# Kernel tuning notes

Hardware: AMD Instinct MI355X
Metric: run time of the kernel (lower is better)

The kernel has to match this reference:

```python
import jax, jax.numpy as jnp
import numpy as np
from jax import lax

B, T, N, E, H = 8, 12, 716, 10, 64
DIN = 1 + H  # GCN input dim = x(1) concat state(H)
CS = 1       # conv_steps (predict_time)


def setup_inputs() -> dict:
    key = jax.random.key(0)
    ks = jax.random.split(key, 26)
    def rn(i, shape, s=0.1):
        return jax.random.normal(ks[i], shape, jnp.float32) * s
    data = jax.random.normal(ks[0], (B, T, N, 1), jnp.float32)
    tid = jax.random.uniform(ks[1], (B, T, N, 1), jnp.float32)          # time-of-day in [0,1)
    diw = jax.random.randint(ks[2], (B, T, N, 1), 0, 7).astype(jnp.float32)  # day-of-week
    source = jnp.concatenate([data, tid, diw], axis=-1)
    return dict(
        source=source,
        node_embeddings=rn(3, (N, E), 1.0),
        tid_emb=rn(4, (288, E), 1.0),
        diw_emb=rn(5, (7, E), 1.0),
        wp_g=rn(6, (2, E, 2, DIN, 2 * H)),
        bp_g=rn(7, (2, E, 2 * H)),
        fc1W_g=rn(8, (2, 16, DIN)), fc1b_g=rn(9, (2, 16)),
        fc2W_g=rn(10, (2, 2, 16)), fc2b_g=rn(11, (2, 2)),
        fc3W_g=rn(12, (2, E, 2)), fc3b_g=rn(13, (2, E)),
        wp_u=rn(14, (2, E, 2, DIN, H)),
        bp_u=rn(15, (2, E, H)),
        fc1W_u=rn(16, (2, 16, DIN)), fc1b_u=rn(17, (2, 16)),
        fc2W_u=rn(18, (2, 2, 16)), fc2b_u=rn(19, (2, 2)),
        fc3W_u=rn(20, (2, E, 2)), fc3b_u=rn(21, (2, E)),
        predW=rn(22, (2, T, CS, H)),
        predB=rn(23, (2, T)),
        skipW=rn(24, (T, CS, H)),
        skipB=rn(25, (T,)),
    )


def _gcn(x, emb_t, static, wp, bp, fc):
    # x: [B,N,DIN], emb_t: [B,N,E], static: [N,E]
    fc1W, fc1b, fc2W, fc2b, fc3W, fc3b = fc
    h = jax.nn.sigmoid(x @ fc1W.T + fc1b)
    h = jax.nn.sigmoid(h @ fc2W.T + fc2b)
    x_ = h @ fc3W.T + fc3b                            # [B,N,E]
    nodevec = jnp.tanh(emb_t * x_)                    # [B,N,E]
    graph = jax.nn.relu(jnp.einsum('bne,bme->bnm', nodevec, nodevec))
    d = jnp.sum(graph, axis=-1) ** -0.5               # [B,N]
    L = d[:, :, None] * graph * d[:, None, :]         # D^-1/2 A D^-1/2 support
    xg2 = jnp.einsum('bnm,bmc->bnc', L, x)
    w = jnp.einsum('ne,ekio->nkio', static, wp)       # [N,2,DIN,out]
    b = static @ bp                                   # [N,out]
    # support1 is identity -> x_g1 == x
    return (jnp.einsum('bni,nio->bno', x, w[:, 0])
            + jnp.einsum('bni,nio->bno', xg2, w[:, 1]) + b)


def _gru_layer(x_seq, emb_seq, static, gate_p, upd_p):
    # x_seq: [T,B,N,1], emb_seq: [T,B,N,E]
    wp_g, bp_g, fc_g = gate_p
    wp_u, bp_u, fc_u = upd_p
    Hd = wp_u.shape[-1]
    def step(state, inp):
        x, emb = inp
        xs = jnp.concatenate([x, state], axis=-1)
        zr = jax.nn.sigmoid(_gcn(xs, emb, static, wp_g, bp_g, fc_g))
        z, r = jnp.split(zr, 2, axis=-1)
        cand = jnp.concatenate([x, z * state], axis=-1)
        hc = jnp.tanh(_gcn(cand, emb, static, wp_u, bp_u, fc_u))
        h = r * state + (1 - r) * hc
        return h, h
    h0 = jnp.zeros(x_seq.shape[1:3] + (Hd,), x_seq.dtype)
    _, hs = lax.scan(step, h0, (x_seq, emb_seq))
    return hs  # [T,B,N,H]


def reference(source, node_embeddings, tid_emb, diw_emb,
              wp_g, bp_g, fc1W_g, fc1b_g, fc2W_g, fc2b_g, fc3W_g, fc3b_g,
              wp_u, bp_u, fc1W_u, fc1b_u, fc2W_u, fc2b_u, fc3W_u, fc3b_u,
              predW, predB, skipW, skipB):
    x = source[..., :1]                                   # [B,T,N,1]
    tid_idx = (source[..., 1] * 288).astype(jnp.int32)
    diw_idx = source[..., 2].astype(jnp.int32)
    emb = node_embeddings * tid_emb[tid_idx] * diw_emb[diw_idx]  # [B,T,N,E]
    x_t = jnp.moveaxis(x, 1, 0)                           # [T,B,N,1]
    emb_t = jnp.moveaxis(emb, 1, 0)                       # [T,B,N,E]
    cur = x_t
    predict = jnp.zeros((x.shape[0], T, x.shape[2], 1), x.dtype)
    for c in range(2):  # two structurally distinct GRU layers
        gate_p = (wp_g[c], bp_g[c], (fc1W_g[c], fc1b_g[c], fc2W_g[c], fc2b_g[c], fc3W_g[c], fc3b_g[c]))
        upd_p = (wp_u[c], bp_u[c], (fc1W_u[c], fc1b_u[c], fc2W_u[c], fc2b_u[c], fc3W_u[c], fc3b_u[c]))
        hs = _gru_layer(cur, emb_t, node_embeddings, gate_p, upd_p)
        ci = jnp.moveaxis(hs[-CS:], 0, 1)                 # [B,CS,N,H] (dropout is identity in eval)
        out = jnp.einsum('bcnh,och->bon', ci, predW[c]) + predB[c][None, :, None]
        predict = predict + out[..., None]                # [B,T,N,1]
        if c == 0:
            sk = jnp.einsum('bcnh,och->bon', ci, skipW) + skipB[None, :, None]
            cur = x_t - jnp.moveaxis(sk[..., None], 1, 0)
    return predict
```

## Files before the change

### kernel.cpp

```cpp
#include <hip/hip_runtime.h>
#include <math.h>

#define BB 8
#define TT 12
#define NN 716
#define EE 10
#define HH 64
#define DIN 65
#define OG 128
#define OU 64
#define XSP 68
#define JS 12
#define JRX 60
#define NTN 128
#define NP 768
#define NI4 17

__device__ __forceinline__ float sigmf(float x){ return 1.0f/(1.0f+__expf(-x)); }

__global__ void k_emb(const float* __restrict__ src, const float* __restrict__ ne,
                      const float* __restrict__ te, const float* __restrict__ de,
                      float* __restrict__ emb, float* __restrict__ cur){
  int idx = blockIdx.x*256 + threadIdx.x;
  if (idx >= BB*TT*NN) return;
  int n = idx % NN; int t = (idx/NN) % TT; int b = idx/(NN*TT);
  const float* s = src + (size_t)idx*3;
  float x = s[0];
  int ti = (int)(s[1]*288.0f);
  int di = (int)(s[2]);
  size_t eo = ((size_t)b*TT + t)*NN*EE + (size_t)n*EE;
  #pragma unroll
  for (int e=0;e<EE;e++)
    emb[eo+e] = ne[n*EE+e]*te[ti*EE+e]*de[di*EE+e];
  cur[((size_t)t*BB + b)*NN + n] = x;
}

__global__ __launch_bounds__(256) void k_prep_w4m(
    const float* __restrict__ ne, const float* __restrict__ wp_g,
    const float* __restrict__ wp_u, float* __restrict__ wg4,
    float* __restrict__ wu4)
{
  __shared__ float wps[EE*4*OG];
  int which = blockIdx.z;
  const float* wp = which ? wp_u : wp_g;
  float* w4 = which ? wu4 : wg4;
  int O = which ? OU : OG;
  int ki4 = blockIdx.x;
  int nq  = blockIdx.y;
  int k = ki4/NI4, i4 = ki4 - k*NI4;
  int tid = threadIdx.x;
  for (int idx=tid; idx<EE*4*O; idx+=256){
    int e = idx/(4*O); int rem = idx - e*4*O; int sub = rem/O; int o = rem - sub*O;
    int i = i4*4 + sub;
    wps[idx] = (i<DIN) ? wp[(((size_t)e*2+k)*DIN+i)*O + o] : 0.f;
  }
  __syncthreads();
  int NG = 256/O;
  int o = tid & (O-1), ng = tid / O;
  int n1 = nq*179, n2 = min(NN, n1+179);
  for (int n = n1+ng; n < n2; n += NG){
    float4 a = {0.f,0.f,0.f,0.f};
    #pragma unroll
    for (int e=0;e<EE;e++){
      float nef = ne[n*EE+e];
      a.x += nef*wps[e*4*O + 0*O + o];
      a.y += nef*wps[e*4*O + 1*O + o];
      a.z += nef*wps[e*4*O + 2*O + o];
      a.w += nef*wps[e*4*O + 3*O + o];
    }
    ((float4*)w4)[((size_t)(n*2+k)*NI4 + i4)*O + o] = a;
  }
}

__global__ void k_misc(const float* __restrict__ ne,
                       const float* __restrict__ bp_g, const float* __restrict__ bp_u,
                       float* __restrict__ bg, float* __restrict__ bu,
                       float* __restrict__ h, const float* __restrict__ cur_c,
                       const float* __restrict__ f1W, const float* __restrict__ f1b,
                       const float* __restrict__ f2W, const float* __restrict__ f2b,
                       const float* __restrict__ f3W, const float* __restrict__ f3b,
                       const float* __restrict__ emb,
                       float* __restrict__ xsg, float* __restrict__ nv){
  int mt = blockIdx.x*256 + threadIdx.x;
  int MT = gridDim.x*256;
  for (int i=mt; i<BB*NN*HH; i+=MT) h[i] = 0.f;
  for (int i=mt; i<NN*OG; i+=MT){
    int o=i&(OG-1), n=i>>7; float a=0.f;
    #pragma unroll
    for (int e=0;e<EE;e++) a += ne[n*EE+e]*bp_g[e*OG+o];
    bg[i]=a;
  }
  for (int i=mt; i<NN*OU; i+=MT){
    int o=i&(OU-1), n=i>>6; float a=0.f;
    #pragma unroll
    for (int e=0;e<EE;e++) a += ne[n*EE+e]*bp_u[e*OU+o];
    bu[i]=a;
  }
  for (int idx=mt; idx<BB*NN; idx+=MT){
    int b=idx/NN, n=idx-b*NN;
    float x = cur_c[(size_t)b*NN + n];
    float* xr = xsg + (size_t)idx*XSP;
    xr[0]=x;
    #pragma unroll
    for (int i2=1;i2<XSP;i2++) xr[i2]=0.f;
    float h1[16];
    #pragma unroll
    for (int k=0;k<16;k++) h1[k]=sigmf(f1b[k]+f1W[k*DIN]*x);
    float h2[2];
    #pragma unroll
    for (int k=0;k<2;k++){
      float s=f2b[k];
      #pragma unroll
      for (int q=0;q<16;q++) s+=f2W[k*16+q]*h1[q];
      h2[k]=sigmf(s);
    }
    #pragma unroll
    for (int e=0;e<EE;e++){
      float xe=f3b[e]+f3W[e*2]*h2[0]+f3W[e*2+1]*h2[1];
      nv[(size_t)idx*EE+e]=tanhf(emb[(((size_t)b*TT+0)*NN+n)*EE+e]*xe);
    }
  }
}

__global__ __launch_bounds__(256) void k_xg2d(
    const float* __restrict__ nv, const float* __restrict__ xs,
    float* __restrict__ parts, float* __restrict__ dout)
{
  __shared__ float a_nv[NTN*11];
  __shared__ float b_nv[64*11];
  __shared__ float dls[64];
  __shared__ __align__(16) float big[12800];
  float* nvs = big;
  float (*xss)[XSP] = (float(*)[XSP])big;
  float (*gs)[NTN+4] = (float(*)[NTN+4])(big + 4352);

  int nc = blockIdx.x, js = blockIdx.y, b = blockIdx.z;
  int tid = threadIdx.x;
  int n0 = nc*NTN;
  int j0 = js*JRX;
  int jend = min(NN, j0+JRX);
  int cnt = jend - j0;
  {
    const float4* src4 = (const float4*)(nv + (size_t)b*NN*EE);
    for (int i=tid; i<NN*EE/4; i+=256) ((float4*)nvs)[i] = src4[i];
  }
  __syncthreads();
  for (int idx=tid; idx<NTN*EE; idx+=256){
    int r = idx/EE, e = idx - r*EE;
    int n = n0 + r;
    a_nv[r*11+e] = (n<NN) ? nvs[n*EE+e] : 0.f;
  }
  for (int idx=tid; idx<64*EE; idx+=256){
    int r = idx/EE, e = idx - r*EE;
    b_nv[r*11+e] = (r<cnt) ? nvs[(j0+r)*EE+e] : 0.f;
  }
  {
    int jg = tid>>4, ns = tid&15;
    float bv[4][EE];
    #pragma unroll
    for (int r=0;r<4;r++){
      int jr = jg*4+r;
      bool ok = (jr < cnt);
      #pragma unroll
      for (int e=0;e<EE;e++) bv[r][e] = ok ? nvs[(j0+jr)*EE+e] : 0.f;
    }
    float sums[4]={0.f,0.f,0.f,0.f};
    for (int n=ns; n<NN; n+=16){
      float av[EE];
      #pragma unroll
      for (int e=0;e<EE;e++) av[e] = nvs[n*EE+e];
      #pragma unroll
      for (int r=0;r<4;r++){
        float s=0.f;
        #pragma unroll
        for (int e=0;e<EE;e++) s += bv[r][e]*av[e];
        sums[r] += fmaxf(s,0.f);
      }
    }
    #pragma unroll
    for (int r=0;r<4;r++){
      float s = sums[r];
      s += __shfl_xor(s,1,64); s += __shfl_xor(s,2,64);
      s += __shfl_xor(s,4,64); s += __shfl_xor(s,8,64);
      sums[r] = s;
    }
    if (ns==0){
      #pragma unroll
      for (int r=0;r<4;r++){
        int jr = jg*4+r;
        if (jr < cnt){
          float dv = rsqrtf(sums[r]);
          dls[jr] = dv;
          dout[b*NN + j0 + jr] = dv;
        }
      }
    }
  }
  __syncthreads();
  for (int idx=tid; idx<64*64; idx+=256){
    int r = idx>>6, ii = idx&63;
    xss[r][ii] = (r<cnt) ? dls[r]*xs[((size_t)b*NN+j0+r)*XSP+ii] : 0.f;
  }
  if (tid < 64)
    xss[tid][64] = (tid<cnt) ? dls[tid]*xs[((size_t)b*NN+j0+tid)*XSP+64] : 0.f;
  {
    int jg = tid>>4, ng3 = tid&15;
    float g[4][8];
    #pragma unroll
    for (int r=0;r<4;r++)
      #pragma unroll
      for (int s2=0;s2<8;s2++) g[r][s2]=0.f;
    #pragma unroll
    for (int e=0;e<EE;e++){
      float bv[4], av[8];
      #pragma unroll
      for (int r=0;r<4;r++) bv[r] = b_nv[(jg*4+r)*11+e];
      #pragma unroll
      for (int s2=0;s2<8;s2++) av[s2] = a_nv[(ng3*8+s2)*11+e];
      #pragma unroll
      for (int r=0;r<4;r++)
        #pragma unroll
        for (int s2=0;s2<8;s2++) g[r][s2] += bv[r]*av[s2];
    }
    #pragma unroll
    for (int r=0;r<4;r++){
      float4 v0 = { fmaxf(g[r][0],0.f), fmaxf(g[r][1],0.f),
                    fmaxf(g[r][2],0.f), fmaxf(g[r][3],0.f) };
      float4 v1 = { fmaxf(g[r][4],0.f), fmaxf(g[r][5],0.f),
                    fmaxf(g[r][6],0.f), fmaxf(g[r][7],0.f) };
      *(float4*)&gs[jg*4+r][ng3*8]   = v0;
      *(float4*)&gs[jg*4+r][ng3*8+4] = v1;
    }
  }
  __syncthreads();
  int ng = tid >> 3, ig = tid & 7;
  float acc[4][8];
  #pragma unroll
  for (int r=0;r<4;r++)
    #pragma unroll
    for (int s2=0;s2<8;s2++) acc[r][s2]=0.f;
  for (int jj=0; jj<cnt; ++jj){
    float4 g4  = *(const float4*)&gs[jj][ng*4];
    float4 x4a = *(const float4*)&xss[jj][ig*8];
    float4 x4b = *(const float4*)&xss[jj][ig*8+4];
    float gr[4] = {g4.x, g4.y, g4.z, g4.w};
    float xr[8] = {x4a.x,x4a.y,x4a.z,x4a.w, x4b.x,x4b.y,x4b.z,x4b.w};
    #pragma unroll
    for (int r=0;r<4;r++)
      #pragma unroll
      for (int s2=0;s2<8;s2++) acc[r][s2] += gr[r]*xr[s2];
  }
  #pragma unroll
  for (int r=0;r<4;r++){
    int n = n0 + ng*4 + r;
    float4 v0 = { acc[r][0], acc[r][1], acc[r][2], acc[r][3] };
    float4 v1 = { acc[r][4], acc[r][5], acc[r][6], acc[r][7] };
    size_t base = (((size_t)js*BB+b)*NP+n)*XSP;
    *(float4*)&parts[base + ig*8]     = v0;
    *(float4*)&parts[base + ig*8 + 4] = v1;
  }
  if (tid < NTN){
    float s = 0.f;
    for (int jj=0; jj<cnt; ++jj) s += gs[jj][tid]*xss[jj][64];
    parts[(((size_t)js*BB+b)*NP + n0+tid)*XSP + 64] = s;
  }
}

__global__ __launch_bounds__(256, 4) void k_tr_gate(
    const float* __restrict__ wg, const float* __restrict__ bg,
    const float* __restrict__ parts, const float* __restrict__ d,
    const float* __restrict__ xsg,
    const float* __restrict__ cur_ct, const float* __restrict__ h,
    const float* __restrict__ emb, int t,
    const float* __restrict__ f1W, const float* __restrict__ f1b,
    const float* __restrict__ f2W, const float* __restrict__ f2b,
    const float* __restrict__ f3W, const float* __restrict__ f3b,
    float* __restrict__ rbuf, float* __restrict__ xsu, float* __restrict__ nv)
{
  __shared__ float xg2s[BB][XSP];
  __shared__ float xss[BB][XSP];
  __shared__ float cs[BB][DIN];
  __shared__ float h1s[BB][16];
  __shared__ float h2s[BB][2];
  int n = blockIdx.x;
  int tid = threadIdx.x;
  for (int idx=tid; idx<BB*XSP; idx+=256){
    int b = idx/XSP, i = idx - b*XSP;
    float s = 0.f;
    if (i < 65){
      #pragma unroll
      for (int js2=0; js2<JS; js2++)
        s += parts[(((size_t)js2*BB+b)*NP+n)*XSP + i];
      s *= d[b*NN+n];
    }
    xg2s[b][i] = s;
  }
  for (int idx=tid; idx<BB*XSP; idx+=256){
    int b = idx/XSP, i = idx - b*XSP;
    xss[b][i] = (i<65) ? xsg[((size_t)b*NN+n)*XSP + i] : 0.f;
  }
  __syncthreads();
  {
    int o = tid & 127, half = tid >> 7;
    const float4* w0p = (const float4*)wg + ((size_t)n*2+0)*NI4*OG + o;
    const float4* w1p = w0p + (size_t)NI4*OG;
    float bgv = bg[n*OG+o];
    float acc[4]; acc[0]=bgv; acc[1]=bgv; acc[2]=bgv; acc[3]=bgv;
    #pragma unroll 2
    for (int i4=0;i4<NI4;i4++){
      float4 w0 = w0p[(size_t)i4*OG];
      float4 w1 = w1p[(size_t)i4*OG];
      int i = i4*4;
      #pragma unroll
      for (int bb=0;bb<4;bb++){
        int b = 2*bb+half;
        acc[bb] += xss[b][i]*w0.x + xss[b][i+1]*w0.y
                 + xss[b][i+2]*w0.z + xss[b][i+3]*w0.w
                 + xg2s[b][i]*w1.x + xg2s[b][i+1]*w1.y
                 + xg2s[b][i+2]*w1.z + xg2s[b][i+3]*w1.w;
      }
    }
    #pragma unroll
    for (int bb=0;bb<4;bb++){
      int b = 2*bb+half;
      float v = sigmf(acc[bb]);
      if (o < 64){
        float cv = v * h[((size_t)b*NN+n)*HH + o];
        xsu[((size_t)b*NN+n)*XSP + 1 + o] = cv;
        cs[b][1+o] = cv;
      } else {
        rbuf[((size_t)b*NN+n)*HH + (o-64)] = v;
      }
    }
    if (o == 64){
      #pragma unroll
      for (int bb=0;bb<4;bb++){
        int b = 2*bb+half;
        float x = cur_ct[(size_t)b*NN+n];
        cs[b][0] = x;
        xsu[((size_t)b*NN+n)*XSP] = x;
      }
    }
  }
  __syncthreads();
  if (tid < BB*16){
    int b=tid>>4, k=tid&15;
    const float* wr = f1W + k*DIN;
    float s = f1b[k];
    #pragma unroll
    for (int i=0;i<DIN;i++) s += cs[b][i]*wr[i];
    h1s[b][k] = sigmf(s);
  }
  __syncthreads();
  if (tid < BB*2){
    int b=tid>>1, k=tid&1;
    float s = f2b[k];
    #pragma unroll
    for (int q2=0;q2<16;q2++) s += h1s[b][q2]*f2W[k*16+q2];
    h2s[b][k] = sigmf(s);
  }
  __syncthreads();
  if (tid < BB*EE){
    int b=tid/EE, e=tid-b*EE;
    float xe = f3b[e] + f3W[e*2]*h2s[b][0] + f3W[e*2+1]*h2s[b][1];
    nv[((size_t)b*NN+n)*EE+e] = tanhf(emb[(((size_t)b*TT+t)*NN+n)*EE+e]*xe);
  }
}

__global__ __launch_bounds__(256, 4) void k_tr_upd(
    const float* __restrict__ wu, const float* __restrict__ bu,
    const float* __restrict__ parts, const float* __restrict__ d,
    const float* __restrict__ xsu,
    const float* __restrict__ rbuf, float* __restrict__ h,
    float* __restrict__ cur, int c, int t,
    const float* __restrict__ emb,
    const float* __restrict__ f1W, const float* __restrict__ f1b,
    const float* __restrict__ f2W, const float* __restrict__ f2b,
    const float* __restrict__ f3W, const float* __restrict__ f3b,
    float* __restrict__ xsg, float* __restrict__ nv,
    const float* __restrict__ predW, const float* __restrict__ predB,
    const float* __restrict__ skipW, const float* __restrict__ skipB,
    float* __restrict__ out)
{
  __shared__ float xg2s[BB][XSP];
  __shared__ float xss[BB][XSP];
  __shared__ float hs[BB][HH];
  __shared__ float h1s[BB][16];
  __shared__ float h2s[BB][2];
  __shared__ float xns[BB];
  int n = blockIdx.x;
  int tid = threadIdx.x;
  for (int idx=tid; idx<BB*XSP; idx+=256){
    int b = idx/XSP, i = idx - b*XSP;
    float s = 0.f;
    if (i < 65){
      #pragma unroll
      for (int js2=0; js2<JS; js2++)
        s += parts[(((size_t)js2*BB+b)*NP+n)*XSP + i];
      s *= d[b*NN+n];
    }
    xg2s[b][i] = s;
  }
  for (int idx=tid; idx<BB*XSP; idx+=256){
    int b = idx/XSP, i = idx - b*XSP;
    xss[b][i] = (i<65) ? xsu[((size_t)b*NN+n)*XSP + i] : 0.f;
  }
  __syncthreads();
  {
    int o = tid & 63, grp = tid >> 6;
    const float4* w0p = (const float4*)wu + ((size_t)n*2+0)*NI4*OU + o;
    const float4* w1p = w0p + (size_t)NI4*OU;
    float acc[2];
    acc[0] = bu[n*OU+o]; acc[1] = acc[0];
    #pragma unroll 2
    for (int i4=0;i4<NI4;i4++){
      float4 w0 = w0p[(size_t)i4*OU];
      float4 w1 = w1p[(size_t)i4*OU];
      int i = i4*4;
      #pragma unroll
      for (int bb=0;bb<2;bb++){
        int b = grp + 4*bb;
        acc[bb] += xss[b][i]*w0.x + xss[b][i+1]*w0.y
                 + xss[b][i+2]*w0.z + xss[b][i+3]*w0.w
                 + xg2s[b][i]*w1.x + xg2s[b][i+1]*w1.y
                 + xg2s[b][i+2]*w1.z + xg2s[b][i+3]*w1.w;
      }
    }
    #pragma unroll
    for (int bb=0;bb<2;bb++){
      int b = grp + 4*bb;
      float hc = tanhf(acc[bb]);
      float r = rbuf[((size_t)b*NN+n)*HH+o];
      float hold = h[((size_t)b*NN+n)*HH+o];
      float hn = r*hold + (1.f-r)*hc;
      h[((size_t)b*NN+n)*HH+o] = hn;
      hs[b][o] = hn;
    }
  }
  __syncthreads();
  if (t < TT-1){
    if (tid < BB){
      float x = cur[(((size_t)c*TT + (t+1))*BB + tid)*NN + n];
      xns[tid] = x;
      xsg[((size_t)tid*NN+n)*XSP] = x;
    }
    for (int idx=tid; idx<BB*HH; idx+=256){
      int b = idx>>6, oo = idx&63;
      xsg[((size_t)b*NN+n)*XSP + 1 + oo] = hs[b][oo];
    }
    __syncthreads();
    if (tid < BB*16){
      int b=tid>>4, k=tid&15;
      const float* wr = f1W + k*DIN;
      float s = f1b[k] + wr[0]*xns[b];
      #pragma unroll
      for (int oo=0;oo<HH;oo++) s += hs[b][oo]*wr[1+oo];
      h1s[b][k] = sigmf(s);
    }
    __syncthreads();
    if (tid < BB*2){
      int b=tid>>1, k=tid&1;
      float s = f2b[k];
      #pragma unroll
      for (int q2=0;q2<16;q2++) s += h1s[b][q2]*f2W[k*16+q2];
      h2s[b][k] = sigmf(s);
    }
    __syncthreads();
    if (tid < BB*EE){
      int b=tid/EE, e=tid-b*EE;
      float xe = f3b[e] + f3W[e*2]*h2s[b][0] + f3W[e*2+1]*h2s[b][1];
      nv[((size_t)b*NN+n)*EE+e] =
        tanhf(emb[(((size_t)b*TT+(t+1))*NN+n)*EE+e]*xe);
    }
  } else {
    if (tid < BB*TT){
      int b = tid/TT, ot = tid - b*TT;
      const float* pw = predW + ((size_t)c*TT + ot)*HH;
      float pv = predB[c*TT+ot];
      #pragma unroll
      for (int q2=0;q2<HH;q2++) pv += hs[b][q2]*pw[q2];
      size_t oi = ((size_t)b*TT+ot)*NN + n;
      if (c == 0){
        out[oi] = pv;
        const float* sw = skipW + (size_t)ot*HH;
        float sk = skipB[ot];
        #pragma unroll
        for (int q2=0;q2<HH;q2++) sk += hs[b][q2]*sw[q2];
        cur[(((size_t)TT+ot)*BB + b)*NN + n] =
            cur[((size_t)ot*BB + b)*NN + n] - sk;
      } else {
        out[oi] += pv;
      }
    }
  }
}

extern "C" void kernel_launch(void* const* d_in, const int* in_sizes, int n_in,
                              void* d_out, int out_size, void* d_ws, size_t ws_size,
                              hipStream_t stream){
  const float* src  = (const float*)d_in[0];
  const float* ne   = (const float*)d_in[1];
  const float* te   = (const float*)d_in[2];
  const float* de   = (const float*)d_in[3];
  const float* wp_g = (const float*)d_in[4];
  const float* bp_g = (const float*)d_in[5];
  const float* f1W_g= (const float*)d_in[6];
  const float* f1b_g= (const float*)d_in[7];
  const float* f2W_g= (const float*)d_in[8];
  const float* f2b_g= (const float*)d_in[9];
  const float* f3W_g= (const float*)d_in[10];
  const float* f3b_g= (const float*)d_in[11];
  const float* wp_u = (const float*)d_in[12];
  const float* bp_u = (const float*)d_in[13];
  const float* f1W_u= (const float*)d_in[14];
  const float* f1b_u= (const float*)d_in[15];
  const float* f2W_u= (const float*)d_in[16];
  const float* f2b_u= (const float*)d_in[17];
  const float* f3W_u= (const float*)d_in[18];
  const float* f3b_u= (const float*)d_in[19];
  const float* predW= (const float*)d_in[20];
  const float* predB= (const float*)d_in[21];
  const float* skipW= (const float*)d_in[22];
  const float* skipB= (const float*)d_in[23];

  float* ws   = (float*)d_ws;
  float* emb  = ws;
  float* cur  = emb  + (size_t)BB*TT*NN*EE;
  float* wg   = cur  + (size_t)2*TT*BB*NN;
  float* bg   = wg   + (size_t)NN*2*NI4*OG*4;
  float* wu   = bg   + (size_t)NN*OG;
  float* bu   = wu   + (size_t)NN*2*NI4*OU*4;
  float* h    = bu   + (size_t)NN*OU;
  float* xsg  = h    + (size_t)BB*NN*HH;
  float* xsu  = xsg  + (size_t)BB*NN*XSP;
  float* nv   = xsu  + (size_t)BB*NN*XSP;
  float* dbuf = nv   + (size_t)BB*NN*EE;
  float* parts= dbuf + (size_t)BB*NN;
  float* rbuf = parts+ (size_t)JS*BB*NP*XSP;
  float* outp = (float*)d_out;

  k_emb<<<(BB*TT*NN+255)/256, 256, 0, stream>>>(src, ne, te, de, emb, cur);

  for (int c=0;c<2;c++){
    k_prep_w4m<<<dim3(2*NI4,4,2),256,0,stream>>>(ne,
        wp_g + (size_t)c*EE*2*DIN*OG, wp_u + (size_t)c*EE*2*DIN*OU, wg, wu);
    k_misc<<<1024,256,0,stream>>>(ne, bp_g + (size_t)c*EE*OG, bp_u + (size_t)c*EE*OU,
        bg, bu, h, cur + (size_t)c*TT*BB*NN,
        f1W_g + c*16*DIN, f1b_g + c*16, f2W_g + c*32, f2b_g + c*2,
        f3W_g + c*EE*2, f3b_g + c*EE, emb, xsg, nv);
    for (int t=0;t<TT;t++){
      k_xg2d<<<dim3(6,JS,BB),256,0,stream>>>(nv, xsg, parts, dbuf);
      k_tr_gate<<<NN,256,0,stream>>>(wg, bg, parts, dbuf, xsg,
          cur + ((size_t)c*TT+t)*BB*NN, h, emb, t,
          f1W_u + c*16*DIN, f1b_u + c*16, f2W_u + c*32, f2b_u + c*2,
          f3W_u + c*EE*2, f3b_u + c*EE, rbuf, xsu, nv);
      k_xg2d<<<dim3(6,JS,BB),256,0,stream>>>(nv, xsu, parts, dbuf);
      k_tr_upd<<<NN,256,0,stream>>>(wu, bu, parts, dbuf, xsu, rbuf, h,
          cur, c, t, emb,
          f1W_g + c*16*DIN, f1b_g + c*16, f2W_g + c*32, f2b_g + c*2,
          f3W_g + c*EE*2, f3b_g + c*EE,
          xsg, nv, predW, predB, skipW, skipB, outp);
    }
  }
}
```

Baseline: 3.217 ms.

## Restructure adjacency kernel to loop n-chunks per block and dedupe degree sums

The normalized-adjacency aggregation kernel now assigns one block per (j-slice, batch) and loops over the six node chunks internally. Degree sums are computed once per j-slice instead of being recomputed by each node-chunk block. Embedding rows are padded to 12 floats for vectorized shared loads. The j-split grows from 12 to 32 slices, which reduces the grid to 256 blocks and increases the partial-sum traffic read back by the gate and update kernels.

```diff
diff --git a/kernel.cpp b/kernel.cpp
--- a/kernel.cpp
+++ b/kernel.cpp
@@ -10,11 +10,12 @@
 #define OG 128
 #define OU 64
 #define XSP 68
-#define JS 12
-#define JRX 60
+#define JS 32
+#define JRX 23
 #define NTN 128
 #define NP 768
 #define NI4 17
+#define NVP 12
 
 __device__ __forceinline__ float sigmf(float x){ return 1.0f/(1.0f+__expf(-x)); }
 
@@ -126,49 +127,48 @@
     const float* __restrict__ nv, const float* __restrict__ xs,
     float* __restrict__ parts, float* __restrict__ dout)
 {
-  __shared__ float a_nv[NTN*11];
-  __shared__ float b_nv[64*11];
-  __shared__ float dls[64];
-  __shared__ __align__(16) float big[12800];
-  float* nvs = big;
-  float (*xss)[XSP] = (float(*)[XSP])big;
-  float (*gs)[NTN+4] = (float(*)[NTN+4])(big + 4352);
-
-  int nc = blockIdx.x, js = blockIdx.y, b = blockIdx.z;
+  __shared__ __align__(16) float nvs[NN*NVP];
+  __shared__ __align__(16) float xss[32][XSP];
+  __shared__ __align__(16) float gs[32][NTN+4];
+  __shared__ float dls[32];
+  int js = blockIdx.x, b = blockIdx.y;
   int tid = threadIdx.x;
-  int n0 = nc*NTN;
   int j0 = js*JRX;
-  int jend = min(NN, j0+JRX);
-  int cnt = jend - j0;
+  int cnt = NN - j0; if (cnt > JRX) cnt = JRX;
   {
-    const float4* src4 = (const float4*)(nv + (size_t)b*NN*EE);
-    for (int i=tid; i<NN*EE/4; i+=256) ((float4*)nvs)[i] = src4[i];
-  }
-  __syncthreads();
-  for (int idx=tid; idx<NTN*EE; idx+=256){
-    int r = idx/EE, e = idx - r*EE;
-    int n = n0 + r;
-    a_nv[r*11+e] = (n<NN) ? nvs[n*EE+e] : 0.f;
-  }
-  for (int idx=tid; idx<64*EE; idx+=256){
-    int r = idx/EE, e = idx - r*EE;
-    b_nv[r*11+e] = (r<cnt) ? nvs[(j0+r)*EE+e] : 0.f;
+    const float* nvb = nv + (size_t)b*NN*EE;
+    for (int idx=tid; idx<NN*EE; idx+=256){
+      int n = idx/10, e = idx - n*10;
+      nvs[n*NVP+e] = nvb[idx];
+    }
+  }
+  __syncthreads();
+  int jg = tid>>5, ns = tid&31;
+  float bv[4][EE];
+  #pragma unroll
+  for (int r=0;r<4;r++){
+    int jr = jg*4+r;
+    if (jr < cnt){
+      const float* bp2 = &nvs[(j0+jr)*NVP];
+      float4 b0 = *(const float4*)bp2;
+      float4 b1 = *(const float4*)(bp2+4);
+      float2 b2 = *(const float2*)(bp2+8);
+      bv[r][0]=b0.x; bv[r][1]=b0.y; bv[r][2]=b0.z; bv[r][3]=b0.w;
+      bv[r][4]=b1.x; bv[r][5]=b1.y; bv[r][6]=b1.z; bv[r][7]=b1.w;
+      bv[r][8]=b2.x; bv[r][9]=b2.y;
+    } else {
+      #pragma unroll
+      for (int e=0;e<EE;e++) bv[r][e]=0.f;
+    }
   }
   {
-    int jg = tid>>4, ns = tid&15;
-    float bv[4][EE];
-    #pragma unroll
-    for (int r=0;r<4;r++){
-      int jr = jg*4+r;
-      bool ok = (jr < cnt);
-      #pragma unroll
-      for (int e=0;e<EE;e++) bv[r][e] = ok ? nvs[(j0+jr)*EE+e] : 0.f;
-    }
     float sums[4]={0.f,0.f,0.f,0.f};
-    for (int n=ns; n<NN; n+=16){
-      float av[EE];
-      #pragma unroll
-      for (int e=0;e<EE;e++) av[e] = nvs[n*EE+e];
+    for (int n=ns; n<NN; n+=32){
+      const float* ap = &nvs[n*NVP];
+      float4 a0 = *(const float4*)ap;
+      float4 a1 = *(const float4*)(ap+4);
+      float2 a2 = *(const float2*)(ap+8);
+      float av[10] = {a0.x,a0.y,a0.z,a0.w,a1.x,a1.y,a1.z,a1.w,a2.x,a2.y};
       #pragma unroll
       for (int r=0;r<4;r++){
         float s=0.f;
@@ -182,6 +182,7 @@
       float s = sums[r];
       s += __shfl_xor(s,1,64); s += __shfl_xor(s,2,64);
       s += __shfl_xor(s,4,64); s += __shfl_xor(s,8,64);
+      s += __shfl_xor(s,16,64);
       sums[r] = s;
     }
     if (ns==0){
@@ -197,72 +198,80 @@
     }
   }
   __syncthreads();
-  for (int idx=tid; idx<64*64; idx+=256){
-    int r = idx>>6, ii = idx&63;
-    xss[r][ii] = (r<cnt) ? dls[r]*xs[((size_t)b*NN+j0+r)*XSP+ii] : 0.f;
-  }
-  if (tid < 64)
-    xss[tid][64] = (tid<cnt) ? dls[tid]*xs[((size_t)b*NN+j0+tid)*XSP+64] : 0.f;
-  {
-    int jg = tid>>4, ng3 = tid&15;
-    float g[4][8];
-    #pragma unroll
-    for (int r=0;r<4;r++)
-      #pragma unroll
-      for (int s2=0;s2<8;s2++) g[r][s2]=0.f;
-    #pragma unroll
-    for (int e=0;e<EE;e++){
-      float bv[4], av[8];
-      #pragma unroll
-      for (int r=0;r<4;r++) bv[r] = b_nv[(jg*4+r)*11+e];
-      #pragma unroll
-      for (int s2=0;s2<8;s2++) av[s2] = a_nv[(ng3*8+s2)*11+e];
+  for (int idx=tid; idx<32*XSP; idx+=256){
+    int r = idx/XSP, ii = idx - r*XSP;
+    float v = 0.f;
+    if (r < cnt && ii <= 64)
+      v = dls[r]*xs[((size_t)b*NN+j0+r)*XSP + ii];
+    xss[r][ii] = v;
+  }
+  int ng = tid >> 3, ig = tid & 7;
+  int ng4 = tid & 31;
+  for (int nc=0; nc<6; ++nc){
+    int n0 = nc*NTN;
+    {
+      float g[4][4];
+      #pragma unroll
+      for (int r=0;r<4;r++){ g[r][0]=0;g[r][1]=0;g[r][2]=0;g[r][3]=0; }
+      #pragma unroll
+      for (int s2=0;s2<4;s2++){
+        int n = n0 + ng4*4 + s2;
+        if (n < NN){
+          const float* ap = &nvs[n*NVP];
+          float4 a0 = *(const float4*)ap;
+          float4 a1 = *(const float4*)(ap+4);
+          float2 a2 = *(const float2*)(ap+8);
+          float av[10] = {a0.x,a0.y,a0.z,a0.w,a1.x,a1.y,a1.z,a1.w,a2.x,a2.y};
+          #pragma unroll
+          for (int r=0;r<4;r++){
+            float s=0.f;
+            #pragma unroll
+            for (int e=0;e<EE;e++) s += bv[r][e]*av[e];
+            g[r][s2] = s;
+          }
+        }
+      }
+      #pragma unroll
+      for (int r=0;r<4;r++){
+        float4 v = { fmaxf(g[r][0],0.f), fmaxf(g[r][1],0.f),
+                     fmaxf(g[r][2],0.f), fmaxf(g[r][3],0.f) };
+        *(float4*)&gs[jg*4+r][ng4*4] = v;
+      }
+    }
+    __syncthreads();
+    {
+      float acc[4][8];
       #pragma unroll
       for (int r=0;r<4;r++)
         #pragma unroll
-        for (int s2=0;s2<8;s2++) g[r][s2] += bv[r]*av[s2];
-    }
-    #pragma unroll
-    for (int r=0;r<4;r++){
-      float4 v0 = { fmaxf(g[r][0],0.f), fmaxf(g[r][1],0.f),
-                    fmaxf(g[r][2],0.f), fmaxf(g[r][3],0.f) };
-      float4 v1 = { fmaxf(g[r][4],0.f), fmaxf(g[r][5],0.f),
-                    fmaxf(g[r][6],0.f), fmaxf(g[r][7],0.f) };
-      *(float4*)&gs[jg*4+r][ng3*8]   = v0;
-      *(float4*)&gs[jg*4+r][ng3*8+4] = v1;
-    }
-  }
-  __syncthreads();
-  int ng = tid >> 3, ig = tid & 7;
-  float acc[4][8];
-  #pragma unroll
-  for (int r=0;r<4;r++)
-    #pragma unroll
-    for (int s2=0;s2<8;s2++) acc[r][s2]=0.f;
-  for (int jj=0; jj<cnt; ++jj){
-    float4 g4  = *(const float4*)&gs[jj][ng*4];
-    float4 x4a = *(const float4*)&xss[jj][ig*8];
-    float4 x4b = *(const float4*)&xss[jj][ig*8+4];
-    float gr[4] = {g4.x, g4.y, g4.z, g4.w};
-    float xr[8] = {x4a.x,x4a.y,x4a.z,x4a.w, x4b.x,x4b.y,x4b.z,x4b.w};
-    #pragma unroll
-    for (int r=0;r<4;r++)
-      #pragma unroll
-      for (int s2=0;s2<8;s2++) acc[r][s2] += gr[r]*xr[s2];
-  }
-  #pragma unroll
-  for (int r=0;r<4;r++){
-    int n = n0 + ng*4 + r;
-    float4 v0 = { acc[r][0], acc[r][1], acc[r][2], acc[r][3] };
-    float4 v1 = { acc[r][4], acc[r][5], acc[r][6], acc[r][7] };
-    size_t base = (((size_t)js*BB+b)*NP+n)*XSP;
-    *(float4*)&parts[base + ig*8]     = v0;
-    *(float4*)&parts[base + ig*8 + 4] = v1;
-  }
-  if (tid < NTN){
-    float s = 0.f;
-    for (int jj=0; jj<cnt; ++jj) s += gs[jj][tid]*xss[jj][64];
-    parts[(((size_t)js*BB+b)*NP + n0+tid)*XSP + 64] = s;
+        for (int s2=0;s2<8;s2++) acc[r][s2]=0.f;
+      for (int jj=0; jj<cnt; ++jj){
+        float4 g4  = *(const float4*)&gs[jj][ng*4];
+        float4 x4a = *(const float4*)&xss[jj][ig*8];
+        float4 x4b = *(const float4*)&xss[jj][ig*8+4];
+        float gr[4] = {g4.x, g4.y, g4.z, g4.w};
+        float xr[8] = {x4a.x,x4a.y,x4a.z,x4a.w, x4b.x,x4b.y,x4b.z,x4b.w};
+        #pragma unroll
+        for (int r=0;r<4;r++)
+          #pragma unroll
+          for (int s2=0;s2<8;s2++) acc[r][s2] += gr[r]*xr[s2];
+      }
+      #pragma unroll
+      for (int r=0;r<4;r++){
+        int n = n0 + ng*4 + r;
+        float4 v0 = { acc[r][0], acc[r][1], acc[r][2], acc[r][3] };
+        float4 v1 = { acc[r][4], acc[r][5], acc[r][6], acc[r][7] };
+        size_t base = (((size_t)js*BB+b)*NP+n)*XSP;
+        *(float4*)&parts[base + ig*8]     = v0;
+        *(float4*)&parts[base + ig*8 + 4] = v1;
+      }
+      if (tid < NTN){
+        float s = 0.f;
+        for (int jj=0; jj<cnt; ++jj) s += gs[jj][tid]*xss[jj][64];
+        parts[(((size_t)js*BB+b)*NP + n0+tid)*XSP + 64] = s;
+      }
+    }
+    __syncthreads();
   }
 }
 
@@ -288,7 +297,7 @@
     int b = idx/XSP, i = idx - b*XSP;
     float s = 0.f;
     if (i < 65){
-      #pragma unroll
+      #pragma unroll 8
       for (int js2=0; js2<JS; js2++)
         s += parts[(((size_t)js2*BB+b)*NP+n)*XSP + i];
       s *= d[b*NN+n];
@@ -394,7 +403,7 @@
     int b = idx/XSP, i = idx - b*XSP;
     float s = 0.f;
     if (i < 65){
-      #pragma unroll
+      #pragma unroll 8
       for (int js2=0; js2<JS; js2++)
         s += parts[(((size_t)js2*BB+b)*NP+n)*XSP + i];
       s *= d[b*NN+n];
@@ -549,12 +558,12 @@
         f1W_g + c*16*DIN, f1b_g + c*16, f2W_g + c*32, f2b_g + c*2,
         f3W_g + c*EE*2, f3b_g + c*EE, emb, xsg, nv);
     for (int t=0;t<TT;t++){
-      k_xg2d<<<dim3(6,JS,BB),256,0,stream>>>(nv, xsg, parts, dbuf);
+      k_xg2d<<<dim3(JS,BB),256,0,stream>>>(nv, xsg, parts, dbuf);
       k_tr_gate<<<NN,256,0,stream>>>(wg, bg, parts, dbuf, xsg,
           cur + ((size_t)c*TT+t)*BB*NN, h, emb, t,
           f1W_u + c*16*DIN, f1b_u + c*16, f2W_u + c*32, f2b_u + c*2,
           f3W_u + c*EE*2, f3b_u + c*EE, rbuf, xsu, nv);
-      k_xg2d<<<dim3(6,JS,BB),256,0,stream>>>(nv, xsu, parts, dbuf);
+      k_xg2d<<<dim3(JS,BB),256,0,stream>>>(nv, xsu, parts, dbuf);
       k_tr_upd<<<NN,256,0,stream>>>(wu, bu, parts, dbuf, xsu, rbuf, h,
           cur, c, t, emb,
           f1W_g + c*16*DIN, f1b_g + c*16, f2W_g + c*32, f2b_g + c*2,
```

New measurement: 2.968 ms. -7.8%, faster.
